# Kernel tuning notes

Hardware: AMD Instinct MI355X
Metric: run time of the kernel (lower is better)

## Reference

```python
import jax, jax.numpy as jnp
import numpy as np

B, S, H = 4, 2048, 3072
NQ, NKV, D = 16, 8, 256
NEG = -2.3819763e38  # large negative for masking


def setup_inputs() -> dict:
    key = jax.random.key(0)
    ks = jax.random.split(key, 8)
    hidden_states = jax.random.normal(ks[0], (B, S, H), dtype=jnp.float32)
    # rotary frequencies: angle theta per (pos, dim-pair), Gemma-style base 10000
    inv_freq = 1.0 / (10000.0 ** (np.arange(0, D, 2, dtype=np.float32) / D))  # [D/2]
    t = np.arange(S, dtype=np.float32)
    ang = np.outer(t, inv_freq)  # [S, D/2]
    freqs_cos = jnp.broadcast_to(jnp.asarray(np.cos(ang)), (B, S, D // 2)).astype(jnp.float32)
    freqs_sin = jnp.broadcast_to(jnp.asarray(np.sin(ang)), (B, S, D // 2)).astype(jnp.float32)
    # additive causal mask [B,1,S,S]
    causal = jnp.tril(jnp.ones((S, S), dtype=bool))
    mask = jnp.where(causal, 0.0, NEG).astype(jnp.float32)[None, None]
    mask = jnp.broadcast_to(mask, (B, 1, S, S))
    sc = 0.02
    wq = jax.random.normal(ks[1], (NQ * D, H), dtype=jnp.float32) * sc
    wk = jax.random.normal(ks[2], (NKV * D, H), dtype=jnp.float32) * sc
    wv = jax.random.normal(ks[3], (NKV * D, H), dtype=jnp.float32) * sc
    wo = jax.random.normal(ks[4], (H, NQ * D), dtype=jnp.float32) * sc
    return {"hidden_states": hidden_states, "freqs_cos": freqs_cos,
            "freqs_sin": freqs_sin, "mask": mask,
            "wq": wq, "wk": wk, "wv": wv, "wo": wo}


def _apply_rotary(x, cos, sin):
    # x: [B,S,N,Dh]; cos/sin: [B,S,Dh/2]. Complex rotation: (x1 + i x2) * (cos + i sin)
    d2 = x.shape[-1] // 2
    x1, x2 = x[..., :d2], x[..., d2:]
    c = cos[:, :, None, :]
    s = sin[:, :, None, :]
    return jnp.concatenate([x1 * c - x2 * s, x1 * s + x2 * c], axis=-1)


def reference(hidden_states, freqs_cos, freqs_sin, mask, wq, wk, wv, wo):
    b, s, _ = hidden_states.shape
    scaling = D ** -0.5
    xq = (hidden_states @ wq.T).reshape(b, s, NQ, D)
    xk = (hidden_states @ wk.T).reshape(b, s, NKV, D)
    xv = (hidden_states @ wv.T).reshape(b, s, NKV, D)
    xq = _apply_rotary(xq, freqs_cos, freqs_sin)
    xk = _apply_rotary(xk, freqs_cos, freqs_sin)
    # GQA: repeat kv heads to match query heads
    g = NQ // NKV
    xk = jnp.repeat(xk, g, axis=2)  # [b,s,NQ,D]
    xv = jnp.repeat(xv, g, axis=2)
    scores = jnp.einsum('bqhd,bkhd->bhqk', xq * scaling, xk) + mask
    probs = jax.nn.softmax(scores, axis=-1)
    out = jnp.einsum('bhqk,bkhd->bqhd', probs, xv).reshape(b, s, NQ * D)
    return out @ wo.T
```

## Files before the change

kernel.cpp:

```cpp
#include <hip/hip_runtime.h>

#define DEVI __device__ __forceinline__

typedef __attribute__((ext_vector_type(8))) short s16x8;
typedef __attribute__((ext_vector_type(4))) float f32x4;
typedef unsigned short u16;

DEVI u16 f2bf(float f){
  unsigned u = __float_as_uint(f);
  u += 0x7FFFu + ((u >> 16) & 1u);
  return (u16)(u >> 16);
}
DEVI float bf2f(u16 s){ return __uint_as_float(((unsigned)s) << 16); }

DEVI void gload16(const void* g, void* l){
  __builtin_amdgcn_global_load_lds((const __attribute__((address_space(1))) void*)g,
                                   (__attribute__((address_space(3))) void*)l, 16, 0, 0);
}

__global__ __launch_bounds__(256) void cast_bf16_kernel(const float* __restrict__ src,
                                                        u16* __restrict__ dst, int n4){
  int i = blockIdx.x*256 + threadIdx.x;
  if (i < n4){
    float4 v = reinterpret_cast<const float4*>(src)[i];
    ushort4 o;
    o.x = f2bf(v.x); o.y = f2bf(v.y); o.z = f2bf(v.z); o.w = f2bf(v.w);
    reinterpret_cast<ushort4*>(dst)[i] = o;
  }
}

__global__ __launch_bounds__(256) void rope_kernel(u16* __restrict__ X,
                                                   const float* __restrict__ fc,
                                                   const float* __restrict__ fs, int NH){
  int tid = blockIdx.x*256 + threadIdx.x;
  int rr = tid >> 4;
  int d0 = (tid & 15) * 8;
  int s  = rr & 2047;
  int b  = (rr >> 11) / NH;
  size_t base = (size_t)rr * 256;
  s16x8 x1 = *(const s16x8*)&X[base + d0];
  s16x8 x2 = *(const s16x8*)&X[base + 128 + d0];
  const float* cp = fc + ((size_t)(b*2048 + s))*128 + d0;
  const float* sp = fs + ((size_t)(b*2048 + s))*128 + d0;
  alignas(16) u16 o1[8], o2[8];
  #pragma unroll
  for (int j=0;j<8;j++){
    float c = cp[j], sn = sp[j];
    float a = bf2f((u16)x1[j]);
    float bb = bf2f((u16)x2[j]);
    o1[j] = f2bf(a*c - bb*sn);
    o2[j] = f2bf(a*sn + bb*c);
  }
  *(s16x8*)&X[base + d0]       = *(const s16x8*)o1;
  *(s16x8*)&X[base + 128 + d0] = *(const s16x8*)o2;
}

template<int MODE>
__global__ __launch_bounds__(512,2) void gemm256_kernel(
    const u16* __restrict__ A, const u16* __restrict__ Bw,
    int K, int nbn, int Nn,
    float* __restrict__ Cf, u16* __restrict__ Qo, u16* __restrict__ Ko, u16* __restrict__ Vo)
{
  __shared__ u16 LDSb[4][16384];
  const int nwg = gridDim.x;
  const int bid0 = blockIdx.x;
  const int bid = (bid0 & 7)*(nwg >> 3) + (bid0 >> 3);
  const int bm = bid / nbn, bn = bid % nbn;
  const int t = threadIdx.x, ln = t&63;
  const int wvid = t>>6;
  const int wr = wvid>>2, wc = wvid&3;
  const int frow = ln&15, g = ln>>4;
  const int NT = K >> 5;

  int arow[2], acol[2];
  #pragma unroll
  for (int i=0;i<2;i++){
    const int ci = i*512 + t;
    const int L = (ci*16) ^ (((ci>>3)&7)<<4);
    arow[i] = L >> 6;
    acol[i] = (L & 63) >> 1;
  }
  const u16* Apan = A  + (size_t)(bm*256)*K;
  const u16* Bpan = Bw + (size_t)(bn*256)*K;

  int aoff[8], boff[4];
  #pragma unroll
  for (int mi=0;mi<8;mi++){
    const int m = wr*128 + mi*16 + frow;
    const int L = m*64 + g*16;
    aoff[mi] = L ^ (((m>>1)&7)<<4);
  }
  #pragma unroll
  for (int ni=0;ni<4;ni++){
    const int n = wc*64 + ni*16 + frow;
    const int L = n*64 + g*16;
    boff[ni] = 16384 + (L ^ (((n>>1)&7)<<4));
  }

  f32x4 acc[8][4];
  #pragma unroll
  for (int i=0;i<8;i++)
    #pragma unroll
    for (int j=0;j<4;j++) acc[i][j] = f32x4{0.f,0.f,0.f,0.f};

  auto stageA = [&](int T){
    char* base = (char*)&LDSb[T&3][0];
    const size_t kk = (size_t)T*32;
    #pragma unroll
    for (int i=0;i<2;i++){
      const int ci = i*512 + t;
      gload16(Apan + (size_t)arow[i]*K + kk + acol[i], base + (ci & ~63)*16);
    }
  };
  auto stageB = [&](int T){
    char* base = (char*)&LDSb[T&3][0] + 16384;
    const size_t kk = (size_t)T*32;
    #pragma unroll
    for (int i=0;i<2;i++){
      const int ci = i*512 + t;
      gload16(Bpan + (size_t)arow[i]*K + kk + acol[i], base + (ci & ~63)*16);
    }
  };

  stageA(0); stageB(0);
  stageA(1); stageB(1);
  stageA(2); stageB(2);
  asm volatile("s_waitcnt vmcnt(8)" ::: "memory");
  __builtin_amdgcn_s_barrier();

  for (int T=0; T<NT; ++T){
    const char* sb = (const char*)&LDSb[T&3][0];
    s16x8 af[8], bfr[4];
    #pragma unroll
    for (int mi=0;mi<4;mi++) af[mi] = *(const s16x8*)(sb + aoff[mi]);
    #pragma unroll
    for (int ni=0;ni<4;ni++) bfr[ni] = *(const s16x8*)(sb + boff[ni]);
    if (T+3 < NT) stageA(T+3);
    __builtin_amdgcn_sched_barrier(0);
    __builtin_amdgcn_s_barrier();
    __builtin_amdgcn_s_setprio(1);
    #pragma unroll
    for (int mi=0;mi<4;mi++)
      #pragma unroll
      for (int ni=0;ni<4;ni++)
        acc[mi][ni] = __builtin_amdgcn_mfma_f32_16x16x32_bf16(af[mi], bfr[ni], acc[mi][ni], 0,0,0);
    __builtin_amdgcn_s_setprio(0);
    __builtin_amdgcn_sched_barrier(0);
    __builtin_amdgcn_s_barrier();
    #pragma unroll
    for (int mi=4;mi<8;mi++) af[mi] = *(const s16x8*)(sb + aoff[mi]);
    if (T+3 < NT) stageB(T+3);
    __builtin_amdgcn_sched_barrier(0);
    __builtin_amdgcn_s_barrier();
    __builtin_amdgcn_s_setprio(1);
    #pragma unroll
    for (int mi=4;mi<8;mi++)
      #pragma unroll
      for (int ni=0;ni<4;ni++)
        acc[mi][ni] = __builtin_amdgcn_mfma_f32_16x16x32_bf16(af[mi], bfr[ni], acc[mi][ni], 0,0,0);
    __builtin_amdgcn_s_setprio(0);
    __builtin_amdgcn_sched_barrier(0);
    if (T < NT-3)       asm volatile("s_waitcnt vmcnt(8)" ::: "memory");
    else if (T == NT-3) asm volatile("s_waitcnt vmcnt(4)" ::: "memory");
    else if (T == NT-2) asm volatile("s_waitcnt vmcnt(0)" ::: "memory");
    __builtin_amdgcn_s_barrier();
  }

  const int mbase = bm*256 + wr*128;
  const int nbase = bn*256 + wc*64;
  #pragma unroll
  for (int mi=0;mi<8;mi++){
    #pragma unroll
    for (int ni=0;ni<4;ni++){
      #pragma unroll
      for (int r=0;r<4;r++){
        const int m = mbase + mi*16 + g*4 + r;
        const int n = nbase + ni*16 + frow;
        if (MODE == 0){
          const int b = m >> 11, s = m & 2047;
          const u16 v = f2bf(acc[mi][ni][r]);
          if (n < 4096){
            const int h = n >> 8, d = n & 255;
            Qo[((((size_t)b*16 + h)*2048 + s) << 8) + d] = v;
          } else if (n < 6144){
            const int n2 = n - 4096; const int h = n2 >> 8, d = n2 & 255;
            Ko[((((size_t)b*8 + h)*2048 + s) << 8) + d] = v;
          } else {
            const int n2 = n - 6144; const int h = n2 >> 8, d = n2 & 255;
            Vo[((((size_t)b*8 + h)*2048 + s) << 8) + d] = v;
          }
        } else {
          Cf[(size_t)m*Nn + n] = acc[mi][ni][r];
        }
      }
    }
  }
}

__global__ __launch_bounds__(512,2) void flash_attn_kernel(
    const u16* __restrict__ Qg, const u16* __restrict__ Kg,
    const u16* __restrict__ Vg, u16* __restrict__ Og)
{
  __shared__ u16 Kl[2][32*256];
  __shared__ u16 Vt[256*40];
  __shared__ u16 Pl[8][16*40];
  const int xb = blockIdx.x;
  const int kvh = blockIdx.y, b = blockIdx.z;
  const int t = threadIdx.x, wvid = t>>6, ln = t&63;
  const int frow = ln&15, g = ln>>4;
  const int qh = kvh*2 + (wvid>>2);
  const u16* Qp = Qg + ((size_t)(b*16 + qh) << 19);
  const u16* Kp = Kg + ((size_t)(b*8 + kvh) << 19);
  const u16* Vp = Vg + ((size_t)(b*8 + kvh) << 19);
  const int vd = t & 255;
  const int vh = (t >> 8) << 4;

  s16x8 ones;
  #pragma unroll
  for (int j=0;j<8;j++) ones[j] = (short)0x3F80;

  #pragma unroll 1
  for (int seg=0; seg<2; seg++){
    const int qb = seg ? (31 - xb) : xb;
    const int q0 = qb*64 + (wvid&3)*16;
    const int ntiles = qb*2 + 2;

    s16x8 aq[8];
    #pragma unroll
    for (int kk=0;kk<8;kk++){
      s16x8 v = *(const s16x8*)&Qp[(size_t)(q0+frow)*256 + kk*32 + g*8];
      #pragma unroll
      for (int j=0;j<8;j++) v[j] = (short)f2bf(bf2f((u16)v[j]) * 0.0625f);
      aq[kk] = v;
    }

    f32x4 accO[16];
    #pragma unroll
    for (int i=0;i<16;i++) accO[i] = f32x4{0.f,0.f,0.f,0.f};
    f32x4 accL = f32x4{0.f,0.f,0.f,0.f};
    float mrow[4] = {-1e30f,-1e30f,-1e30f,-1e30f};

    alignas(16) u16 va[16];

    #pragma unroll
    for (int i=0;i<2;i++){
      const int ci = i*512 + t;
      const int gelem = (ci*8) ^ ((((unsigned)ci>>5)&7)<<3);
      gload16(Kp + gelem, &Kl[0][(ci & ~63)*8]);
    }
    #pragma unroll
    for (int j=0;j<16;j++) va[j] = Vp[(size_t)(vh + j)*256 + vd];
    __syncthreads();
    *(s16x8*)&Vt[vd*40 + vh]     = *(const s16x8*)&va[0];
    *(s16x8*)&Vt[vd*40 + vh + 8] = *(const s16x8*)&va[8];
    __syncthreads();

    for (int kt=0; kt<ntiles; kt++){
      const int kbase = kt*32;
      const bool haveNext = (kt+1 < ntiles);
      if (haveNext){
        const int kb2 = kbase + 32;
        #pragma unroll
        for (int i=0;i<2;i++){
          const int ci = i*512 + t;
          const int gelem = (ci*8) ^ ((((unsigned)ci>>5)&7)<<3);
          gload16(Kp + (size_t)kb2*256 + gelem, &Kl[(kt+1)&1][(ci & ~63)*8]);
        }
        #pragma unroll
        for (int j=0;j<16;j++) va[j] = Vp[(size_t)(kb2 + vh + j)*256 + vd];
      }

      if (kbase <= q0 + 15){
        const char* Kb8 = (const char*)&Kl[kt&1][0];
        f32x4 sc[2];
        sc[0] = f32x4{0.f,0.f,0.f,0.f};
        sc[1] = f32x4{0.f,0.f,0.f,0.f};
        #pragma unroll
        for (int kb=0;kb<2;kb++){
          const int rr = kb*16 + frow;
          const int sw = (rr&7)<<4;
          const int bb = rr*512 + g*16;
          #pragma unroll
          for (int kk=0;kk<8;kk++){
            const s16x8 bk = *(const s16x8*)(Kb8 + ((bb + kk*64) ^ sw));
            sc[kb] = __builtin_amdgcn_mfma_f32_16x16x32_bf16(aq[kk], bk, sc[kb], 0,0,0);
          }
        }
        if (kbase + 31 > q0){
          #pragma unroll
          for (int r=0;r<4;r++){
            const int qrow = q0 + g*4 + r;
            if (kbase + frow > qrow)      sc[0][r] = -1e30f;
            if (kbase + 16 + frow > qrow) sc[1][r] = -1e30f;
          }
        }
        float mx[4];
        #pragma unroll
        for (int r=0;r<4;r++) mx[r] = fmaxf(sc[0][r], sc[1][r]);
        #pragma unroll
        for (int m=1;m<16;m<<=1)
          #pragma unroll
          for (int r=0;r<4;r++)
            mx[r] = fmaxf(mx[r], __shfl_xor(mx[r], m));
        float need = -1.f;
        #pragma unroll
        for (int r=0;r<4;r++) need = fmaxf(need, mx[r] - mrow[r]);
        if (__any(need > 8.0f)){
          #pragma unroll
          for (int r=0;r<4;r++){
            const float mn = fmaxf(mrow[r], mx[r]);
            const float s = __expf(mrow[r] - mn);
            mrow[r] = mn;
            accL[r] *= s;
            #pragma unroll
            for (int nb=0;nb<16;nb++) accO[nb][r] *= s;
          }
        }
        #pragma unroll
        for (int r=0;r<4;r++){
          const float p0 = __expf(sc[0][r] - mrow[r]);
          const float p1 = __expf(sc[1][r] - mrow[r]);
          Pl[wvid][(g*4+r)*40 + frow]      = f2bf(p0);
          Pl[wvid][(g*4+r)*40 + 16 + frow] = f2bf(p1);
        }
        asm volatile("s_waitcnt lgkmcnt(0)" ::: "memory");
        __builtin_amdgcn_sched_barrier(0);
        const s16x8 pf = *(const s16x8*)&Pl[wvid][frow*40 + g*8];
        accL = __builtin_amdgcn_mfma_f32_16x16x32_bf16(pf, ones, accL, 0,0,0);
        #pragma unroll
        for (int nb=0;nb<16;nb++){
          const s16x8 vf = *(const s16x8*)&Vt[(nb*16+frow)*40 + g*8];
          accO[nb] = __builtin_amdgcn_mfma_f32_16x16x32_bf16(pf, vf, accO[nb], 0,0,0);
        }
      }

      __syncthreads();
      if (haveNext){
        *(s16x8*)&Vt[vd*40 + vh]     = *(const s16x8*)&va[0];
        *(s16x8*)&Vt[vd*40 + vh + 8] = *(const s16x8*)&va[8];
      }
      __syncthreads();
    }

    f32x4 rl;
    #pragma unroll
    for (int r=0;r<4;r++) rl[r] = 1.0f / accL[r];
    #pragma unroll
    for (int nb=0;nb<16;nb++)
      #pragma unroll
      for (int r=0;r<4;r++){
        const int qrow = q0 + g*4 + r;
        Og[(((size_t)(b*2048 + qrow)*16 + qh) << 8) + nb*16 + frow] = f2bf(accO[nb][r] * rl[r]);
      }
  }
}

extern "C" void kernel_launch(void* const* d_in, const int* in_sizes, int n_in,
                              void* d_out, int out_size, void* d_ws, size_t ws_size,
                              hipStream_t stream) {
  const float* hidden = (const float*)d_in[0];
  const float* fcos   = (const float*)d_in[1];
  const float* fsin   = (const float*)d_in[2];
  const float* wq = (const float*)d_in[4];
  const float* wk = (const float*)d_in[5];
  const float* wv = (const float*)d_in[6];
  const float* wo = (const float*)d_in[7];
  float* out = (float*)d_out;

  char* ws = (char*)d_ws;
  u16* Xb   = (u16*)(ws);
  u16* Wcat = (u16*)(ws + 50331648);
  u16* Wob  = (u16*)(ws + 100663296);
  u16* Qb   = (u16*)(ws + 125829120);
  u16* Kb   = (u16*)(ws + 192937984);
  u16* Vb   = (u16*)(ws + 226492416);
  u16* AOb  = (u16*)(ws + 260046848);

  cast_bf16_kernel<<<24576, 256, 0, stream>>>(hidden, Xb, 6291456);
  cast_bf16_kernel<<<12288, 256, 0, stream>>>(wq, Wcat,              3145728);
  cast_bf16_kernel<<< 6144, 256, 0, stream>>>(wk, Wcat + 12582912,   1572864);
  cast_bf16_kernel<<< 6144, 256, 0, stream>>>(wv, Wcat + 18874368,   1572864);
  cast_bf16_kernel<<<12288, 256, 0, stream>>>(wo, Wob,               3145728);

  gemm256_kernel<0><<<32*32, 512, 0, stream>>>(Xb, Wcat, 3072, 32, 8192,
                                               nullptr, Qb, Kb, Vb);

  rope_kernel<<<8192, 256, 0, stream>>>(Qb, fcos, fsin, 16);
  rope_kernel<<<4096, 256, 0, stream>>>(Kb, fcos, fsin, 8);

  flash_attn_kernel<<<dim3(16,8,4), 512, 0, stream>>>(Qb, Kb, Vb, AOb);

  gemm256_kernel<1><<<32*12, 512, 0, stream>>>(AOb, Wob, 4096, 12, 3072,
                                               out, nullptr, nullptr, nullptr);
}
```

Measured before the change: 1.074 ms.

## Parametrize GEMM M-tile and use 128-row tiles for output projection; simplify pipeline

The GEMM kernel now takes its M-tile height as a template parameter. The output projection uses 128x256 tiles, doubling its grid from 384 to 768 workgroups so the CUs are better occupied. The main loop is also rewritten: the split A/B staging, the extra intra-iteration barriers and the setprio calls are replaced by a single stage call at the top, then all LDS reads and MFMAs, then one wait. This makes the QKV GEMM's schedule coarser, which may cost some of the overlap between loads and MFMA that the finer interleaving gave.

```diff
diff --git a/kernel.cpp b/kernel.cpp
--- a/kernel.cpp
+++ b/kernel.cpp
@@ -16,6 +16,14 @@
 DEVI void gload16(const void* g, void* l){
   __builtin_amdgcn_global_load_lds((const __attribute__((address_space(1))) void*)g,
                                    (__attribute__((address_space(3))) void*)l, 16, 0, 0);
+}
+
+template<int N> DEVI void vwait(){
+  if constexpr(N==8)      asm volatile("s_waitcnt vmcnt(8)" ::: "memory");
+  else if constexpr(N==6) asm volatile("s_waitcnt vmcnt(6)" ::: "memory");
+  else if constexpr(N==4) asm volatile("s_waitcnt vmcnt(4)" ::: "memory");
+  else if constexpr(N==3) asm volatile("s_waitcnt vmcnt(3)" ::: "memory");
+  else                    asm volatile("s_waitcnt vmcnt(0)" ::: "memory");
 }
 
 __global__ __launch_bounds__(256) void cast_bf16_kernel(const float* __restrict__ src,
@@ -55,13 +63,16 @@
   *(s16x8*)&X[base + 128 + d0] = *(const s16x8*)o2;
 }
 
-template<int MODE>
+template<int MODE, int MI>
 __global__ __launch_bounds__(512,2) void gemm256_kernel(
     const u16* __restrict__ A, const u16* __restrict__ Bw,
     int K, int nbn, int Nn,
     float* __restrict__ Cf, u16* __restrict__ Qo, u16* __restrict__ Ko, u16* __restrict__ Vo)
 {
-  __shared__ u16 LDSb[4][16384];
+  constexpr int ACH = MI/4;
+  constexpr int LPT = ACH + 2;
+  constexpr int SLOT = MI*2048 + 16384;
+  __shared__ u16 LDSb[4][SLOT/2];
   const int nwg = gridDim.x;
   const int bid0 = blockIdx.x;
   const int bid = (bid0 & 7)*(nwg >> 3) + (bid0 >> 3);
@@ -72,21 +83,26 @@
   const int frow = ln&15, g = ln>>4;
   const int NT = K >> 5;
 
-  int arow[2], acol[2];
+  int arowA[ACH], acolA[ACH], arowB[2], acolB[2];
+  #pragma unroll
+  for (int i=0;i<ACH;i++){
+    const int ci = i*512 + t;
+    const int L = (ci*16) ^ (((ci>>3)&7)<<4);
+    arowA[i] = L >> 6;  acolA[i] = (L & 63) >> 1;
+  }
   #pragma unroll
   for (int i=0;i<2;i++){
     const int ci = i*512 + t;
     const int L = (ci*16) ^ (((ci>>3)&7)<<4);
-    arow[i] = L >> 6;
-    acol[i] = (L & 63) >> 1;
-  }
-  const u16* Apan = A  + (size_t)(bm*256)*K;
+    arowB[i] = L >> 6;  acolB[i] = (L & 63) >> 1;
+  }
+  const u16* Apan = A  + (size_t)(bm*(MI*32))*K;
   const u16* Bpan = Bw + (size_t)(bn*256)*K;
 
-  int aoff[8], boff[4];
-  #pragma unroll
-  for (int mi=0;mi<8;mi++){
-    const int m = wr*128 + mi*16 + frow;
+  int aoff[MI], boff[4];
+  #pragma unroll
+  for (int mi=0;mi<MI;mi++){
+    const int m = wr*(MI*16) + mi*16 + frow;
     const int L = m*64 + g*16;
     aoff[mi] = L ^ (((m>>1)&7)<<4);
   }
@@ -94,82 +110,58 @@
   for (int ni=0;ni<4;ni++){
     const int n = wc*64 + ni*16 + frow;
     const int L = n*64 + g*16;
-    boff[ni] = 16384 + (L ^ (((n>>1)&7)<<4));
-  }
-
-  f32x4 acc[8][4];
-  #pragma unroll
-  for (int i=0;i<8;i++)
+    boff[ni] = MI*2048 + (L ^ (((n>>1)&7)<<4));
+  }
+
+  f32x4 acc[MI][4];
+  #pragma unroll
+  for (int i=0;i<MI;i++)
     #pragma unroll
     for (int j=0;j<4;j++) acc[i][j] = f32x4{0.f,0.f,0.f,0.f};
 
-  auto stageA = [&](int T){
+  auto stage = [&](int T){
     char* base = (char*)&LDSb[T&3][0];
     const size_t kk = (size_t)T*32;
     #pragma unroll
+    for (int i=0;i<ACH;i++){
+      const int ci = i*512 + t;
+      gload16(Apan + (size_t)arowA[i]*K + kk + acolA[i], base + (ci & ~63)*16);
+    }
+    char* baseB = base + MI*2048;
+    #pragma unroll
     for (int i=0;i<2;i++){
       const int ci = i*512 + t;
-      gload16(Apan + (size_t)arow[i]*K + kk + acol[i], base + (ci & ~63)*16);
+      gload16(Bpan + (size_t)arowB[i]*K + kk + acolB[i], baseB + (ci & ~63)*16);
     }
   };
-  auto stageB = [&](int T){
-    char* base = (char*)&LDSb[T&3][0] + 16384;
-    const size_t kk = (size_t)T*32;
-    #pragma unroll
-    for (int i=0;i<2;i++){
-      const int ci = i*512 + t;
-      gload16(Bpan + (size_t)arow[i]*K + kk + acol[i], base + (ci & ~63)*16);
-    }
-  };
-
-  stageA(0); stageB(0);
-  stageA(1); stageB(1);
-  stageA(2); stageB(2);
-  asm volatile("s_waitcnt vmcnt(8)" ::: "memory");
+
+  stage(0); stage(1); stage(2);
+  vwait<2*LPT>();
   __builtin_amdgcn_s_barrier();
 
   for (int T=0; T<NT; ++T){
+    if (T+3 < NT) stage(T+3);
     const char* sb = (const char*)&LDSb[T&3][0];
-    s16x8 af[8], bfr[4];
-    #pragma unroll
-    for (int mi=0;mi<4;mi++) af[mi] = *(const s16x8*)(sb + aoff[mi]);
+    s16x8 af[MI], bfr[4];
     #pragma unroll
     for (int ni=0;ni<4;ni++) bfr[ni] = *(const s16x8*)(sb + boff[ni]);
-    if (T+3 < NT) stageA(T+3);
-    __builtin_amdgcn_sched_barrier(0);
-    __builtin_amdgcn_s_barrier();
-    __builtin_amdgcn_s_setprio(1);
-    #pragma unroll
-    for (int mi=0;mi<4;mi++)
+    #pragma unroll
+    for (int mi=0;mi<MI;mi++) af[mi] = *(const s16x8*)(sb + aoff[mi]);
+    #pragma unroll
+    for (int mi=0;mi<MI;mi++)
       #pragma unroll
       for (int ni=0;ni<4;ni++)
         acc[mi][ni] = __builtin_amdgcn_mfma_f32_16x16x32_bf16(af[mi], bfr[ni], acc[mi][ni], 0,0,0);
-    __builtin_amdgcn_s_setprio(0);
-    __builtin_amdgcn_sched_barrier(0);
+    if (T < NT-3)       vwait<2*LPT>();
+    else if (T == NT-3) vwait<LPT>();
+    else if (T == NT-2) vwait<0>();
     __builtin_amdgcn_s_barrier();
-    #pragma unroll
-    for (int mi=4;mi<8;mi++) af[mi] = *(const s16x8*)(sb + aoff[mi]);
-    if (T+3 < NT) stageB(T+3);
-    __builtin_amdgcn_sched_barrier(0);
-    __builtin_amdgcn_s_barrier();
-    __builtin_amdgcn_s_setprio(1);
-    #pragma unroll
-    for (int mi=4;mi<8;mi++)
-      #pragma unroll
-      for (int ni=0;ni<4;ni++)
-        acc[mi][ni] = __builtin_amdgcn_mfma_f32_16x16x32_bf16(af[mi], bfr[ni], acc[mi][ni], 0,0,0);
-    __builtin_amdgcn_s_setprio(0);
-    __builtin_amdgcn_sched_barrier(0);
-    if (T < NT-3)       asm volatile("s_waitcnt vmcnt(8)" ::: "memory");
-    else if (T == NT-3) asm volatile("s_waitcnt vmcnt(4)" ::: "memory");
-    else if (T == NT-2) asm volatile("s_waitcnt vmcnt(0)" ::: "memory");
-    __builtin_amdgcn_s_barrier();
-  }
-
-  const int mbase = bm*256 + wr*128;
+  }
+
+  const int mbase = bm*(MI*32) + wr*(MI*16);
   const int nbase = bn*256 + wc*64;
   #pragma unroll
-  for (int mi=0;mi<8;mi++){
+  for (int mi=0;mi<MI;mi++){
     #pragma unroll
     for (int ni=0;ni<4;ni++){
       #pragma unroll
@@ -382,14 +374,14 @@
   cast_bf16_kernel<<< 6144, 256, 0, stream>>>(wv, Wcat + 18874368,   1572864);
   cast_bf16_kernel<<<12288, 256, 0, stream>>>(wo, Wob,               3145728);
 
-  gemm256_kernel<0><<<32*32, 512, 0, stream>>>(Xb, Wcat, 3072, 32, 8192,
-                                               nullptr, Qb, Kb, Vb);
+  gemm256_kernel<0,8><<<32*32, 512, 0, stream>>>(Xb, Wcat, 3072, 32, 8192,
+                                                 nullptr, Qb, Kb, Vb);
 
   rope_kernel<<<8192, 256, 0, stream>>>(Qb, fcos, fsin, 16);
   rope_kernel<<<4096, 256, 0, stream>>>(Kb, fcos, fsin, 8);
 
   flash_attn_kernel<<<dim3(16,8,4), 512, 0, stream>>>(Qb, Kb, Vb, AOb);
 
-  gemm256_kernel<1><<<32*12, 512, 0, stream>>>(AOb, Wob, 4096, 12, 3072,
-                                               out, nullptr, nullptr, nullptr);
-}
+  gemm256_kernel<1,4><<<64*12, 512, 0, stream>>>(AOb, Wob, 4096, 12, 3072,
+                                                 out, nullptr, nullptr, nullptr);
+}
```

Result: no change. 1.065 ms (-0.9%).

## Restructure GEMM to K=64 tiles with double-buffered half-tile staging in four phases

Applied to the files above, without the earlier changes.

The bf16 GEMM now uses 64-wide K steps with two 64KB LDS buffers instead of four 32-wide buffers. Each step runs four phases, and each phase issues one quarter of the next tiles' global-to-LDS loads, so loads interleave with MFMA work and each barrier covers twice as much compute. The LDS swizzle and offsets are recomputed for 128-byte rows. The risk is higher register pressure from holding B fragments for both k-substeps, a shallower prefetch depth, and an extra lgkmcnt wait in every phase.

```diff
diff --git a/kernel.cpp b/kernel.cpp
--- a/kernel.cpp
+++ b/kernel.cpp
@@ -56,12 +56,12 @@
 }
 
 template<int MODE>
-__global__ __launch_bounds__(512,2) void gemm256_kernel(
+__global__ __launch_bounds__(512,2) void gemm8p_kernel(
     const u16* __restrict__ A, const u16* __restrict__ Bw,
     int K, int nbn, int Nn,
     float* __restrict__ Cf, u16* __restrict__ Qo, u16* __restrict__ Ko, u16* __restrict__ Vo)
 {
-  __shared__ u16 LDSb[4][16384];
+  __shared__ u16 LDSb[2][32768];
   const int nwg = gridDim.x;
   const int bid0 = blockIdx.x;
   const int bid = (bid0 & 7)*(nwg >> 3) + (bid0 >> 3);
@@ -70,31 +70,36 @@
   const int wvid = t>>6;
   const int wr = wvid>>2, wc = wvid&3;
   const int frow = ln&15, g = ln>>4;
-  const int NT = K >> 5;
-
-  int arow[2], acol[2];
+  const int NT = K >> 6;
+
+  size_t soff[2];
   #pragma unroll
   for (int i=0;i<2;i++){
-    const int ci = i*512 + t;
-    const int L = (ci*16) ^ (((ci>>3)&7)<<4);
-    arow[i] = L >> 6;
-    acol[i] = (L & 63) >> 1;
+    const int phys = (i*512 + t)*16;
+    const int L = phys ^ (((phys>>7)&7)<<4);
+    soff[i] = (size_t)(L >> 7) * K + ((L & 127) >> 1);
   }
   const u16* Apan = A  + (size_t)(bm*256)*K;
   const u16* Bpan = Bw + (size_t)(bn*256)*K;
 
-  int aoff[8], boff[4];
+  int aoff[8][2], boff[4][2];
   #pragma unroll
   for (int mi=0;mi<8;mi++){
-    const int m = wr*128 + mi*16 + frow;
-    const int L = m*64 + g*16;
-    aoff[mi] = L ^ (((m>>1)&7)<<4);
+    const int row = mi*16 + frow;
+    #pragma unroll
+    for (int ks=0;ks<2;ks++){
+      const int L = row*128 + ks*64 + g*16;
+      aoff[mi][ks] = wr*16384 + (L ^ ((row&7)<<4));
+    }
   }
   #pragma unroll
   for (int ni=0;ni<4;ni++){
-    const int n = wc*64 + ni*16 + frow;
-    const int L = n*64 + g*16;
-    boff[ni] = 16384 + (L ^ (((n>>1)&7)<<4));
+    const int row = (wc&1)*64 + ni*16 + frow;
+    #pragma unroll
+    for (int ks=0;ks<2;ks++){
+      const int L = row*128 + ks*64 + g*16;
+      boff[ni][ks] = 32768 + (wc>>1)*16384 + (L ^ ((row&7)<<4));
+    }
   }
 
   f32x4 acc[8][4];
@@ -103,67 +108,61 @@
     #pragma unroll
     for (int j=0;j<4;j++) acc[i][j] = f32x4{0.f,0.f,0.f,0.f};
 
-  auto stageA = [&](int T){
-    char* base = (char*)&LDSb[T&3][0];
-    const size_t kk = (size_t)T*32;
-    #pragma unroll
-    for (int i=0;i<2;i++){
-      const int ci = i*512 + t;
-      gload16(Apan + (size_t)arow[i]*K + kk + acol[i], base + (ci & ~63)*16);
-    }
+  auto stageHalf = [&](int buf, int ht, int tstep){
+    char* dst = (char*)&LDSb[buf][0] + ht*16384;
+    const u16* src = (ht < 2 ? Apan : Bpan) + (size_t)((ht&1)*128)*K + (size_t)tstep*64;
+    #pragma unroll
+    for (int i=0;i<2;i++)
+      gload16(src + soff[i], dst + (i*512 + t)*16);
   };
-  auto stageB = [&](int T){
-    char* base = (char*)&LDSb[T&3][0] + 16384;
-    const size_t kk = (size_t)T*32;
-    #pragma unroll
-    for (int i=0;i<2;i++){
-      const int ci = i*512 + t;
-      gload16(Bpan + (size_t)arow[i]*K + kk + acol[i], base + (ci & ~63)*16);
-    }
-  };
-
-  stageA(0); stageB(0);
-  stageA(1); stageB(1);
-  stageA(2); stageB(2);
-  asm volatile("s_waitcnt vmcnt(8)" ::: "memory");
+
+  stageHalf(0,0,0); stageHalf(0,1,0); stageHalf(0,2,0); stageHalf(0,3,0);
+  if (NT > 1){ stageHalf(1,2,1); stageHalf(1,3,1); }
+  asm volatile("s_waitcnt vmcnt(4)" ::: "memory");
   __builtin_amdgcn_s_barrier();
 
   for (int T=0; T<NT; ++T){
-    const char* sb = (const char*)&LDSb[T&3][0];
-    s16x8 af[8], bfr[4];
-    #pragma unroll
-    for (int mi=0;mi<4;mi++) af[mi] = *(const s16x8*)(sb + aoff[mi]);
-    #pragma unroll
-    for (int ni=0;ni<4;ni++) bfr[ni] = *(const s16x8*)(sb + boff[ni]);
-    if (T+3 < NT) stageA(T+3);
-    __builtin_amdgcn_sched_barrier(0);
-    __builtin_amdgcn_s_barrier();
-    __builtin_amdgcn_s_setprio(1);
-    #pragma unroll
-    for (int mi=0;mi<4;mi++)
-      #pragma unroll
-      for (int ni=0;ni<4;ni++)
-        acc[mi][ni] = __builtin_amdgcn_mfma_f32_16x16x32_bf16(af[mi], bfr[ni], acc[mi][ni], 0,0,0);
-    __builtin_amdgcn_s_setprio(0);
-    __builtin_amdgcn_sched_barrier(0);
-    __builtin_amdgcn_s_barrier();
-    #pragma unroll
-    for (int mi=4;mi<8;mi++) af[mi] = *(const s16x8*)(sb + aoff[mi]);
-    if (T+3 < NT) stageB(T+3);
-    __builtin_amdgcn_sched_barrier(0);
-    __builtin_amdgcn_s_barrier();
-    __builtin_amdgcn_s_setprio(1);
-    #pragma unroll
-    for (int mi=4;mi<8;mi++)
-      #pragma unroll
-      for (int ni=0;ni<4;ni++)
-        acc[mi][ni] = __builtin_amdgcn_mfma_f32_16x16x32_bf16(af[mi], bfr[ni], acc[mi][ni], 0,0,0);
-    __builtin_amdgcn_s_setprio(0);
-    __builtin_amdgcn_sched_barrier(0);
-    if (T < NT-3)       asm volatile("s_waitcnt vmcnt(8)" ::: "memory");
-    else if (T == NT-3) asm volatile("s_waitcnt vmcnt(4)" ::: "memory");
-    else if (T == NT-2) asm volatile("s_waitcnt vmcnt(0)" ::: "memory");
-    __builtin_amdgcn_s_barrier();
+    const char* sb = (const char*)&LDSb[T&1][0];
+    s16x8 bh[4][2];
+    #pragma unroll
+    for (int p=0;p<4;++p){
+      if (p==0){
+        #pragma unroll
+        for (int ni=0;ni<4;ni++)
+          #pragma unroll
+          for (int ks=0;ks<2;ks++)
+            bh[ni][ks] = *(const s16x8*)(sb + boff[ni][ks]);
+      }
+      s16x8 afr[2][2];
+      #pragma unroll
+      for (int m2=0;m2<2;m2++)
+        #pragma unroll
+        for (int ks=0;ks<2;ks++)
+          afr[m2][ks] = *(const s16x8*)(sb + aoff[p*2+m2][ks]);
+      if      (p==0){ if (T+1 < NT) stageHalf((T+1)&1, 0, T+1); }
+      else if (p==1){ if (T+1 < NT) stageHalf((T+1)&1, 1, T+1); }
+      else if (p==2){ if (T+2 < NT) stageHalf(T&1,     2, T+2); }
+      else          { if (T+2 < NT) stageHalf(T&1,     3, T+2); }
+      __builtin_amdgcn_s_barrier();
+      asm volatile("s_waitcnt lgkmcnt(0)" ::: "memory");
+      __builtin_amdgcn_sched_barrier(0);
+      __builtin_amdgcn_s_setprio(1);
+      #pragma unroll
+      for (int ks=0;ks<2;ks++)
+        #pragma unroll
+        for (int m2=0;m2<2;m2++)
+          #pragma unroll
+          for (int ni=0;ni<4;ni++)
+            acc[p*2+m2][ni] = __builtin_amdgcn_mfma_f32_16x16x32_bf16(
+                afr[m2][ks], bh[ni][ks], acc[p*2+m2][ni], 0,0,0);
+      __builtin_amdgcn_s_setprio(0);
+      __builtin_amdgcn_sched_barrier(0);
+      if (p==3){
+        if (T+2 < NT)       { asm volatile("s_waitcnt vmcnt(4)" ::: "memory"); }
+        else if (T+2 == NT) { asm volatile("s_waitcnt vmcnt(0)" ::: "memory"); }
+      }
+      __builtin_amdgcn_s_barrier();
+    }
   }
 
   const int mbase = bm*256 + wr*128;
@@ -382,14 +381,14 @@
   cast_bf16_kernel<<< 6144, 256, 0, stream>>>(wv, Wcat + 18874368,   1572864);
   cast_bf16_kernel<<<12288, 256, 0, stream>>>(wo, Wob,               3145728);
 
-  gemm256_kernel<0><<<32*32, 512, 0, stream>>>(Xb, Wcat, 3072, 32, 8192,
-                                               nullptr, Qb, Kb, Vb);
+  gemm8p_kernel<0><<<32*32, 512, 0, stream>>>(Xb, Wcat, 3072, 32, 8192,
+                                              nullptr, Qb, Kb, Vb);
 
   rope_kernel<<<8192, 256, 0, stream>>>(Qb, fcos, fsin, 16);
   rope_kernel<<<4096, 256, 0, stream>>>(Kb, fcos, fsin, 8);
 
   flash_attn_kernel<<<dim3(16,8,4), 512, 0, stream>>>(Qb, Kb, Vb, AOb);
 
-  gemm256_kernel<1><<<32*12, 512, 0, stream>>>(AOb, Wob, 4096, 12, 3072,
-                                               out, nullptr, nullptr, nullptr);
-}
+  gemm8p_kernel<1><<<32*12, 512, 0, stream>>>(AOb, Wob, 4096, 12, 3072,
+                                              out, nullptr, nullptr, nullptr);
+}
```

After: 1.037 ms. 3.4% less time.
